# Optimization experiments

Hardware: AMD Instinct MI355X
Metric: run time of the kernel (lower is better)

The kernel has to match this reference:

```python
import jax, jax.numpy as jnp
import numpy as np

B = 16384
NUM_ITEMS = 1_000_000
NUM_CATS = 1001  # num_categories + 1
USER_DIM = 64
ITEM_DIM = 64
CAT_DIM = 32  # item_embedding_dim // 2
DIM1 = 10000
DIM2 = 10000
DEEP_IN = USER_DIM + ITEM_DIM + CAT_DIM + 2 + 2  # 164
HID = [128, 64, 32]
BN_EPS = 1e-5


def setup_inputs() -> dict:
    key = jax.random.key(0)
    ks = jax.random.split(key, 24)
    inp = {
        'user_embeddings': jax.random.normal(ks[0], (B, USER_DIM), jnp.float32),
        'price_features': jax.random.normal(ks[1], (B, 2), jnp.float32),
        'temporal_features': jax.random.normal(ks[2], (B, 2), jnp.float32),
        'item_emb': jax.random.normal(ks[3], (NUM_ITEMS, ITEM_DIM), jnp.float32) * 0.02,
        'cat_emb': jax.random.normal(ks[4], (NUM_CATS, CAT_DIM), jnp.float32) * 0.02,
        'wide_emb1': jax.random.normal(ks[5], (DIM1, 1), jnp.float32) * 0.02,
        'wide_emb2': jax.random.normal(ks[6], (DIM2, 1), jnp.float32) * 0.02,
        'cross_W': jax.random.normal(ks[7], (DIM1 * DIM2,), jnp.float32) * 0.001,
        'item_ids': jax.random.randint(ks[8], (B,), 0, NUM_ITEMS),
        'category_ids': jax.random.randint(ks[9], (B,), 0, NUM_CATS),
        'wf1': jax.random.randint(ks[10], (B,), 0, DIM1),
        'wf2': jax.random.randint(ks[11], (B,), 0, DIM2),
    }
    dims = [DEEP_IN] + HID + [1]
    for i in range(4):
        fan_in = dims[i]
        inp[f'W{i+1}'] = jax.random.normal(ks[12 + i], (dims[i], dims[i + 1]), jnp.float32) / np.sqrt(fan_in)
        inp[f'b{i+1}'] = jnp.zeros((dims[i + 1],), jnp.float32)
    for i in range(3):  # batch-norm affine params (eval mode, running stats = 0/1)
        inp[f'g{i+1}'] = jnp.ones((HID[i],), jnp.float32)
        inp[f'be{i+1}'] = jnp.zeros((HID[i],), jnp.float32)
    return inp


def _bn(x, g, b):
    # eval-mode BatchNorm1d with running_mean=0, running_var=1
    return x * (g / jnp.sqrt(1.0 + BN_EPS)) + b


def reference(user_embeddings, price_features, temporal_features, item_emb, cat_emb,
              wide_emb1, wide_emb2, cross_W, W1, b1, W2, b2, W3, b3, W4, b4,
              g1, be1, g2, be2, g3, be3, item_ids, category_ids, wf1, wf2):
    # deep component
    x = jnp.concatenate([user_embeddings, item_emb[item_ids], cat_emb[category_ids],
                         price_features, temporal_features], axis=-1)  # [B, 164]
    x = jax.nn.relu(_bn(x @ W1 + b1, g1, be1))
    x = jax.nn.relu(_bn(x @ W2 + b2, g2, be2))
    x = jax.nn.relu(_bn(x @ W3 + b3, g3, be3))
    deep_out = x @ W4 + b4  # [B, 1]
    # wide component: per-feature 1-d embeddings + cross term.
    # one_hot(f1) outer one_hot(f2) flattened then dotted with cross_W is exactly
    # a gather at flat index f1*DIM2 + f2 (same math, no [B, DIM1*DIM2] intermediate).
    wide_out = wide_emb1[wf1] + wide_emb2[wf2]  # [B, 1]
    flat_idx = wf1 * DIM2 + wf2
    wide_out = wide_out + cross_W[flat_idx][:, None]
    return wide_out + deep_out
```

## Files before the change

### kernel.cpp

```cpp
#include <hip/hip_runtime.h>

#define NROWS_PER_BLK 64
#define NTHREADS      512
#define DEEP_IN       164
#define H1            128
#define H2            64
#define H3            32
#define DIM2_C        10000
#define BN_RS         0.99999500003749968750f

#define ARENA_F 14400

__global__ __launch_bounds__(NTHREADS) void wad_fused(
    const float* __restrict__ user, const float* __restrict__ price,
    const float* __restrict__ temporal, const float* __restrict__ item_emb,
    const float* __restrict__ cat_emb, const float* __restrict__ we1,
    const float* __restrict__ we2, const float* __restrict__ crossW,
    const int* __restrict__ item_ids, const int* __restrict__ cat_ids,
    const int* __restrict__ wf1, const int* __restrict__ wf2,
    const float* __restrict__ W1, const float* __restrict__ b1,
    const float* __restrict__ W2, const float* __restrict__ b2,
    const float* __restrict__ W3, const float* __restrict__ b3,
    const float* __restrict__ W4, const float* __restrict__ b4,
    const float* __restrict__ g1, const float* __restrict__ be1,
    const float* __restrict__ g2, const float* __restrict__ be2,
    const float* __restrict__ g3, const float* __restrict__ be3,
    float* __restrict__ out)
{
    __shared__ float arena[ARENA_F];
    float* xs    = arena;
    float* h1s   = arena;
    float* h2s   = arena + 8192;
    float* h3s   = arena + 12288;
    float* wideS = arena + 14336;

    const int tid  = threadIdx.x;
    const int lane = tid & 63;
    const int wave = tid >> 6;
    const int r0   = blockIdx.x * NROWS_PER_BLK;

    const float bn_rs = rsqrtf(1.0f + 1e-5f);

    for (int idx = tid; idx < NROWS_PER_BLK * DEEP_IN; idx += NTHREADS) {
        int r = idx / DEEP_IN;
        int k = idx - r * DEEP_IN;
        int R = r0 + r;
        float v;
        if (k < 64)       v = user[R * 64 + k];
        else if (k < 128) v = item_emb[item_ids[R] * 64 + (k - 64)];
        else if (k < 160) v = cat_emb[cat_ids[R] * 32 + (k - 128)];
        else if (k < 162) v = price[R * 2 + (k - 160)];
        else              v = temporal[R * 2 + (k - 162)];
        xs[idx] = v;
    }
    if (tid < NROWS_PER_BLK) {
        int R = r0 + tid;
        int f1 = wf1[R], f2 = wf2[R];
        wideS[tid] = we1[f1] + we2[f2] + crossW[f1 * DIM2_C + f2];
    }
    __syncthreads();

    const int c0 = __builtin_amdgcn_readfirstlane(wave * 16);
    float acc[16];
#pragma unroll
    for (int n = 0; n < 16; ++n) acc[n] = 0.0f;
    {
        const float* xrow = xs + lane * DEEP_IN;
        for (int kq = 0; kq < DEEP_IN / 4; ++kq) {
            float4 a = *(const float4*)(xrow + kq * 4);
            const float* wbase = W1 + kq * 4 * H1 + c0;
#pragma unroll
            for (int kk = 0; kk < 4; ++kk) {
                float av = ((const float*)&a)[kk];
#pragma unroll
                for (int n = 0; n < 16; ++n) acc[n] += av * wbase[kk * H1 + n];
            }
        }
    }
    __syncthreads();

#pragma unroll
    for (int n = 0; n < 16; n += 4) {
        float4 o;
#pragma unroll
        for (int e = 0; e < 4; ++e) {
            int c = c0 + n + e;
            float z = (acc[n + e] + b1[c]) * (g1[c] * bn_rs) + be1[c];
            ((float*)&o)[e] = fmaxf(z, 0.0f);
        }
        int kc  = (c0 + n) >> 2;
        int kcs = kc ^ (lane & 7);
        *(float4*)(h1s + lane * H1 + kcs * 4) = o;
    }
    __syncthreads();

    const int c02 = __builtin_amdgcn_readfirstlane(wave * 8);
    float acc2[8];
#pragma unroll
    for (int n = 0; n < 8; ++n) acc2[n] = 0.0f;
    for (int kq = 0; kq < H1 / 4; ++kq) {
        int kcs = kq ^ (lane & 7);
        float4 a = *(const float4*)(h1s + lane * H1 + kcs * 4);
        const float* wbase = W2 + kq * 4 * H2 + c02;
#pragma unroll
        for (int kk = 0; kk < 4; ++kk) {
            float av = ((const float*)&a)[kk];
#pragma unroll
            for (int n = 0; n < 8; ++n) acc2[n] += av * wbase[kk * H2 + n];
        }
    }
#pragma unroll
    for (int n = 0; n < 8; n += 4) {
        float4 o;
#pragma unroll
        for (int e = 0; e < 4; ++e) {
            int c = c02 + n + e;
            float z = (acc2[n + e] + b2[c]) * (g2[c] * bn_rs) + be2[c];
            ((float*)&o)[e] = fmaxf(z, 0.0f);
        }
        int kc  = (c02 + n) >> 2;
        int kcs = kc ^ (lane & 7);
        *(float4*)(h2s + lane * H2 + kcs * 4) = o;
    }
    __syncthreads();

    const int c03 = __builtin_amdgcn_readfirstlane(wave * 4);
    float acc3[4];
#pragma unroll
    for (int n = 0; n < 4; ++n) acc3[n] = 0.0f;
    for (int kq = 0; kq < H2 / 4; ++kq) {
        int kcs = kq ^ (lane & 7);
        float4 a = *(const float4*)(h2s + lane * H2 + kcs * 4);
        const float* wbase = W3 + kq * 4 * H3 + c03;
#pragma unroll
        for (int kk = 0; kk < 4; ++kk) {
            float av = ((const float*)&a)[kk];
#pragma unroll
            for (int n = 0; n < 4; ++n) acc3[n] += av * wbase[kk * H3 + n];
        }
    }
    {
        float4 o;
#pragma unroll
        for (int e = 0; e < 4; ++e) {
            int c = c03 + e;
            float z = (acc3[e] + b3[c]) * (g3[c] * bn_rs) + be3[c];
            ((float*)&o)[e] = fmaxf(z, 0.0f);
        }
        int kc  = c03 >> 2;
        int kcs = kc ^ (lane & 7);
        *(float4*)(h3s + lane * H3 + kcs * 4) = o;
    }
    __syncthreads();

    if (tid < NROWS_PER_BLK) {
        int j = tid;
        float s = b4[0];
#pragma unroll
        for (int kq = 0; kq < H3 / 4; ++kq) {
            int kcs = kq ^ (j & 7);
            float4 a = *(const float4*)(h3s + j * H3 + kcs * 4);
#pragma unroll
            for (int e = 0; e < 4; ++e) s += ((const float*)&a)[e] * W4[kq * 4 + e];
        }
        out[r0 + j] = s + wideS[j];
    }
}

extern "C" void kernel_launch(void* const* d_in, const int* in_sizes, int n_in,
                              void* d_out, int out_size, void* d_ws, size_t ws_size,
                              hipStream_t stream) {
    const float* user     = (const float*)d_in[0];
    const float* price    = (const float*)d_in[1];
    const float* temporal = (const float*)d_in[2];
    const float* item_emb = (const float*)d_in[3];
    const float* cat_emb  = (const float*)d_in[4];
    const float* we1      = (const float*)d_in[5];
    const float* we2      = (const float*)d_in[6];
    const float* crossW   = (const float*)d_in[7];
    const int*   item_ids = (const int*)d_in[8];
    const int*   cat_ids  = (const int*)d_in[9];
    const int*   wf1      = (const int*)d_in[10];
    const int*   wf2      = (const int*)d_in[11];
    const float* W1 = (const float*)d_in[12];
    const float* b1 = (const float*)d_in[13];
    const float* W2 = (const float*)d_in[14];
    const float* b2 = (const float*)d_in[15];
    const float* W3 = (const float*)d_in[16];
    const float* b3 = (const float*)d_in[17];
    const float* W4 = (const float*)d_in[18];
    const float* b4 = (const float*)d_in[19];
    const float* g1  = (const float*)d_in[20];
    const float* be1 = (const float*)d_in[21];
    const float* g2  = (const float*)d_in[22];
    const float* be2 = (const float*)d_in[23];
    const float* g3  = (const float*)d_in[24];
    const float* be3 = (const float*)d_in[25];
    float* out = (float*)d_out;

    const int nblocks = 16384 / NROWS_PER_BLK;
    wad_fused<<<nblocks, NTHREADS, 0, stream>>>(
        user, price, temporal, item_emb, cat_emb, we1, we2, crossW,
        item_ids, cat_ids, wf1, wf2,
        W1, b1, W2, b2, W3, b3, W4, b4,
        g1, be1, g2, be2, g3, be3, out);
}
```

Measured before the change: 627.2 us.

## Double block threads, vectorize input gather, and swizzle padded input tile

Raises the block to 1024 threads so each wave computes half as many output columns per layer, which doubles parallelism per row tile. The input staging now loads float4 chunks, including packing price and temporal into one float4, instead of scalar elements, and writes into a padded, XOR-swizzled shared tile to avoid LDS bank conflicts. The activation buffers get separate regions so layer 1 no longer needs the extra barrier that aliasing required. The trade-off is higher register and LDS pressure per block and more redundant weight loads across waves.

```diff
diff --git a/kernel.cpp b/kernel.cpp
--- a/kernel.cpp
+++ b/kernel.cpp
@@ -1,15 +1,21 @@
 #include <hip/hip_runtime.h>
 
-#define NROWS_PER_BLK 64
-#define NTHREADS      512
-#define DEEP_IN       164
-#define H1            128
-#define H2            64
-#define H3            32
-#define DIM2_C        10000
-#define BN_RS         0.99999500003749968750f
-
-#define ARENA_F 14400
+#define NROWS     64
+#define NTHREADS  1024
+#define DEEP_IN   164
+#define NCHUNK    41
+#define XS_STRIDE 192
+#define H1        128
+#define H2        64
+#define H3        32
+#define DIM2_C    10000
+
+#define XS_OFF  0
+#define H1_OFF  (NROWS * XS_STRIDE)
+#define H2_OFF  (H1_OFF + NROWS * H1)
+#define H3_OFF  (H2_OFF + NROWS * H2)
+#define WD_OFF  (H3_OFF + NROWS * H3)
+#define ARENA_F (WD_OFF + NROWS)
 
 __global__ __launch_bounds__(NTHREADS) void wad_fused(
     const float* __restrict__ user, const float* __restrict__ price,
@@ -28,140 +34,137 @@
     float* __restrict__ out)
 {
     __shared__ float arena[ARENA_F];
-    float* xs    = arena;
-    float* h1s   = arena;
-    float* h2s   = arena + 8192;
-    float* h3s   = arena + 12288;
-    float* wideS = arena + 14336;
+    float* xs    = arena + XS_OFF;
+    float* h1s   = arena + H1_OFF;
+    float* h2s   = arena + H2_OFF;
+    float* h3s   = arena + H3_OFF;
+    float* wideS = arena + WD_OFF;
 
     const int tid  = threadIdx.x;
     const int lane = tid & 63;
     const int wave = tid >> 6;
-    const int r0   = blockIdx.x * NROWS_PER_BLK;
+    const int lx   = lane & 7;
+    const int r0   = blockIdx.x * NROWS;
 
     const float bn_rs = rsqrtf(1.0f + 1e-5f);
 
-    for (int idx = tid; idx < NROWS_PER_BLK * DEEP_IN; idx += NTHREADS) {
-        int r = idx / DEEP_IN;
-        int k = idx - r * DEEP_IN;
-        int R = r0 + r;
-        float v;
-        if (k < 64)       v = user[R * 64 + k];
-        else if (k < 128) v = item_emb[item_ids[R] * 64 + (k - 64)];
-        else if (k < 160) v = cat_emb[cat_ids[R] * 32 + (k - 128)];
-        else if (k < 162) v = price[R * 2 + (k - 160)];
-        else              v = temporal[R * 2 + (k - 162)];
-        xs[idx] = v;
-    }
-    if (tid < NROWS_PER_BLK) {
+    for (int idx = tid; idx < NROWS * NCHUNK; idx += NTHREADS) {
+        int r  = idx / NCHUNK;
+        int k4 = idx - r * NCHUNK;
+        int R  = r0 + r;
+        float4 v;
+        if (k4 < 16)      v = *(const float4*)(user + R * 64 + k4 * 4);
+        else if (k4 < 32) v = *(const float4*)(item_emb + item_ids[R] * 64 + (k4 - 16) * 4);
+        else if (k4 < 40) v = *(const float4*)(cat_emb + cat_ids[R] * 32 + (k4 - 32) * 4);
+        else {
+            float2 p = *(const float2*)(price + R * 2);
+            float2 t = *(const float2*)(temporal + R * 2);
+            v = make_float4(p.x, p.y, t.x, t.y);
+        }
+        int kcs = k4 ^ (r & 7);
+        *(float4*)(xs + r * XS_STRIDE + kcs * 4) = v;
+    }
+    if (tid < NROWS) {
         int R = r0 + tid;
         int f1 = wf1[R], f2 = wf2[R];
         wideS[tid] = we1[f1] + we2[f2] + crossW[f1 * DIM2_C + f2];
     }
     __syncthreads();
 
-    const int c0 = __builtin_amdgcn_readfirstlane(wave * 16);
-    float acc[16];
-#pragma unroll
-    for (int n = 0; n < 16; ++n) acc[n] = 0.0f;
     {
-        const float* xrow = xs + lane * DEEP_IN;
-        for (int kq = 0; kq < DEEP_IN / 4; ++kq) {
-            float4 a = *(const float4*)(xrow + kq * 4);
+        const int c0 = __builtin_amdgcn_readfirstlane(wave * 8);
+        float acc[8];
+#pragma unroll
+        for (int n = 0; n < 8; ++n) acc[n] = 0.0f;
+        const float* xrow = xs + lane * XS_STRIDE;
+        for (int kq = 0; kq < NCHUNK; ++kq) {
+            float4 a = *(const float4*)(xrow + (kq ^ lx) * 4);
             const float* wbase = W1 + kq * 4 * H1 + c0;
 #pragma unroll
             for (int kk = 0; kk < 4; ++kk) {
                 float av = ((const float*)&a)[kk];
 #pragma unroll
-                for (int n = 0; n < 16; ++n) acc[n] += av * wbase[kk * H1 + n];
-            }
-        }
-    }
-    __syncthreads();
-
-#pragma unroll
-    for (int n = 0; n < 16; n += 4) {
+                for (int n = 0; n < 8; ++n) acc[n] += av * wbase[kk * H1 + n];
+            }
+        }
+#pragma unroll
+        for (int n = 0; n < 8; n += 4) {
+            float4 o;
+#pragma unroll
+            for (int e = 0; e < 4; ++e) {
+                int c = c0 + n + e;
+                float z = (acc[n + e] + b1[c]) * (g1[c] * bn_rs) + be1[c];
+                ((float*)&o)[e] = fmaxf(z, 0.0f);
+            }
+            int kc  = (c0 + n) >> 2;
+            int kcs = kc ^ lx;
+            *(float4*)(h1s + lane * H1 + kcs * 4) = o;
+        }
+    }
+    __syncthreads();
+
+    {
+        const int c02 = __builtin_amdgcn_readfirstlane(wave * 4);
+        float acc2[4];
+#pragma unroll
+        for (int n = 0; n < 4; ++n) acc2[n] = 0.0f;
+        for (int kq = 0; kq < H1 / 4; ++kq) {
+            float4 a = *(const float4*)(h1s + lane * H1 + (kq ^ lx) * 4);
+            const float* wbase = W2 + kq * 4 * H2 + c02;
+#pragma unroll
+            for (int kk = 0; kk < 4; ++kk) {
+                float av = ((const float*)&a)[kk];
+#pragma unroll
+                for (int n = 0; n < 4; ++n) acc2[n] += av * wbase[kk * H2 + n];
+            }
+        }
         float4 o;
 #pragma unroll
         for (int e = 0; e < 4; ++e) {
-            int c = c0 + n + e;
-            float z = (acc[n + e] + b1[c]) * (g1[c] * bn_rs) + be1[c];
+            int c = c02 + e;
+            float z = (acc2[e] + b2[c]) * (g2[c] * bn_rs) + be2[c];
             ((float*)&o)[e] = fmaxf(z, 0.0f);
         }
-        int kc  = (c0 + n) >> 2;
-        int kcs = kc ^ (lane & 7);
-        *(float4*)(h1s + lane * H1 + kcs * 4) = o;
-    }
-    __syncthreads();
-
-    const int c02 = __builtin_amdgcn_readfirstlane(wave * 8);
-    float acc2[8];
-#pragma unroll
-    for (int n = 0; n < 8; ++n) acc2[n] = 0.0f;
-    for (int kq = 0; kq < H1 / 4; ++kq) {
-        int kcs = kq ^ (lane & 7);
-        float4 a = *(const float4*)(h1s + lane * H1 + kcs * 4);
-        const float* wbase = W2 + kq * 4 * H2 + c02;
-#pragma unroll
-        for (int kk = 0; kk < 4; ++kk) {
-            float av = ((const float*)&a)[kk];
-#pragma unroll
-            for (int n = 0; n < 8; ++n) acc2[n] += av * wbase[kk * H2 + n];
-        }
-    }
-#pragma unroll
-    for (int n = 0; n < 8; n += 4) {
-        float4 o;
-#pragma unroll
-        for (int e = 0; e < 4; ++e) {
-            int c = c02 + n + e;
-            float z = (acc2[n + e] + b2[c]) * (g2[c] * bn_rs) + be2[c];
-            ((float*)&o)[e] = fmaxf(z, 0.0f);
-        }
-        int kc  = (c02 + n) >> 2;
-        int kcs = kc ^ (lane & 7);
+        int kcs = wave ^ lx;
         *(float4*)(h2s + lane * H2 + kcs * 4) = o;
     }
     __syncthreads();
 
-    const int c03 = __builtin_amdgcn_readfirstlane(wave * 4);
-    float acc3[4];
-#pragma unroll
-    for (int n = 0; n < 4; ++n) acc3[n] = 0.0f;
-    for (int kq = 0; kq < H2 / 4; ++kq) {
-        int kcs = kq ^ (lane & 7);
-        float4 a = *(const float4*)(h2s + lane * H2 + kcs * 4);
-        const float* wbase = W3 + kq * 4 * H3 + c03;
-#pragma unroll
-        for (int kk = 0; kk < 4; ++kk) {
-            float av = ((const float*)&a)[kk];
-#pragma unroll
-            for (int n = 0; n < 4; ++n) acc3[n] += av * wbase[kk * H3 + n];
-        }
-    }
     {
-        float4 o;
-#pragma unroll
-        for (int e = 0; e < 4; ++e) {
-            int c = c03 + e;
-            float z = (acc3[e] + b3[c]) * (g3[c] * bn_rs) + be3[c];
-            ((float*)&o)[e] = fmaxf(z, 0.0f);
-        }
-        int kc  = c03 >> 2;
-        int kcs = kc ^ (lane & 7);
-        *(float4*)(h3s + lane * H3 + kcs * 4) = o;
-    }
-    __syncthreads();
-
-    if (tid < NROWS_PER_BLK) {
+        const int c03 = __builtin_amdgcn_readfirstlane(wave * 2);
+        float acc3[2];
+        acc3[0] = 0.0f; acc3[1] = 0.0f;
+        for (int kq = 0; kq < H2 / 4; ++kq) {
+            float4 a = *(const float4*)(h2s + lane * H2 + (kq ^ lx) * 4);
+            const float* wbase = W3 + kq * 4 * H3 + c03;
+#pragma unroll
+            for (int kk = 0; kk < 4; ++kk) {
+                float av = ((const float*)&a)[kk];
+                acc3[0] += av * wbase[kk * H3];
+                acc3[1] += av * wbase[kk * H3 + 1];
+            }
+        }
+        float2 o;
+        {
+            int c = c03;
+            float z0 = (acc3[0] + b3[c]) * (g3[c] * bn_rs) + be3[c];
+            float z1 = (acc3[1] + b3[c + 1]) * (g3[c + 1] * bn_rs) + be3[c + 1];
+            o.x = fmaxf(z0, 0.0f);
+            o.y = fmaxf(z1, 0.0f);
+        }
+        int ps = wave ^ (lane & 15);
+        *(float2*)(h3s + lane * H3 + ps * 2) = o;
+    }
+    __syncthreads();
+
+    if (tid < NROWS) {
         int j = tid;
         float s = b4[0];
 #pragma unroll
-        for (int kq = 0; kq < H3 / 4; ++kq) {
-            int kcs = kq ^ (j & 7);
-            float4 a = *(const float4*)(h3s + j * H3 + kcs * 4);
-#pragma unroll
-            for (int e = 0; e < 4; ++e) s += ((const float*)&a)[e] * W4[kq * 4 + e];
+        for (int w = 0; w < 16; ++w) {
+            int ps = w ^ (j & 15);
+            float2 h = *(const float2*)(h3s + j * H3 + ps * 2);
+            s += h.x * W4[2 * w] + h.y * W4[2 * w + 1];
         }
         out[r0 + j] = s + wideS[j];
     }
@@ -198,7 +201,7 @@
     const float* be3 = (const float*)d_in[25];
     float* out = (float*)d_out;
 
-    const int nblocks = 16384 / NROWS_PER_BLK;
+    const int nblocks = 16384 / NROWS;
     wad_fused<<<nblocks, NTHREADS, 0, stream>>>(
         user, price, temporal, item_emb, cat_emb, we1, we2, crossW,
         item_ids, cat_ids, wf1, wf2,
```

Measured after the change: 616.1 us. About the same (-1.8%).
